# Kernel tuning notes

Measured on AMD Instinct MI355X. Metric: run time of the kernel, lower is better.

## Reference

```python
import jax, jax.numpy as jnp
import numpy as np
from jax import lax

B, S, D = 2, 1024, 1024
N = 16            # mamba state dim
EXPAND = 2
DI = EXPAND * D   # inner dim 2048
K = 4             # depthwise conv kernel
H = 16            # soliton heads
DH = D // H
DT_RANK = D // 16
SOL_DT = 0.1      # soliton integration step


def _ln(x, g, b):
    mu = jnp.mean(x, -1, keepdims=True)
    var = jnp.var(x, -1, keepdims=True)
    return (x - mu) / jnp.sqrt(var + 1e-5) * g + b


def setup_inputs() -> dict:
    key = jax.random.key(0)
    ks = jax.random.split(key, 12)
    def nrm(k, sh, sc=0.02):
        return jax.random.normal(k, sh, jnp.float32) * sc
    return {
        'x': nrm(ks[0], (B, S, D), 1.0),
        'ln1_g': jnp.ones(D), 'ln1_b': jnp.zeros(D),
        'W_in': nrm(ks[1], (D, 2 * DI)), 'b_in': jnp.zeros(2 * DI),
        'conv_w': nrm(ks[2], (DI, K), 0.1), 'conv_b': jnp.zeros(DI),
        'W_xp': nrm(ks[3], (DI, DT_RANK + 2 * N)),
        'W_dt': nrm(ks[4], (DT_RANK, DI), 0.1),
        'b_dt': jnp.full((DI,), -4.6),  # softplus(-4.6) ~ 0.01 init dt
        'A_log': jnp.log(jnp.broadcast_to(jnp.arange(1, N + 1, dtype=jnp.float32), (DI, N))),
        'D_skip': jnp.ones(DI),
        'W_out': nrm(ks[5], (DI, D)), 'b_out': jnp.zeros(D),
        'ln2_g': jnp.ones(D), 'ln2_b': jnp.zeros(D),
        'W_si': nrm(ks[6], (D, D)), 'b_si': jnp.zeros(D),
        'gates': nrm(ks[7], (H, 3), 0.1),   # per-head weights for [sine-Gordon, KdV, Heimburg-Jackson]
        'alpha': nrm(ks[8], (H,), 0.1),     # HJ nonlinearity coefficient
        'W_so': nrm(ks[9], (D, D)), 'b_so': jnp.zeros(D),
    }


def _forward(x, ln1_g, ln1_b, W_in, b_in, conv_w, conv_b, W_xp, W_dt, b_dt,
             A_log, D_skip, W_out, b_out, ln2_g, ln2_b, W_si, b_si,
             gates, alpha, W_so, b_so):
    b, s, d = x.shape
    # ---- Mamba mixer branch ----
    u = _ln(x, ln1_g, ln1_b)
    xz = u @ W_in + b_in                                   # [b,s,2*DI]
    xp, z = jnp.split(xz, 2, axis=-1)                      # [b,s,DI] each
    # causal depthwise conv along sequence
    xt = xp.transpose(0, 2, 1)                             # [b,DI,s]
    yc = lax.conv_general_dilated(xt, conv_w[:, None, :], (1,), [(K - 1, 0)],
                                  feature_group_count=DI,
                                  dimension_numbers=('NCW', 'OIW', 'NCW'))
    xc = jax.nn.silu(yc.transpose(0, 2, 1) + conv_b)       # [b,s,DI]
    dbc = xc @ W_xp
    dtr, Bs, Cs = jnp.split(dbc, [DT_RANK, DT_RANK + N], axis=-1)
    dt = jax.nn.softplus(dtr @ W_dt + b_dt)                # [b,s,DI]
    A = -jnp.exp(A_log)                                    # [DI,N]
    dA = jnp.exp(dt[..., None] * A)                        # [b,s,DI,N]
    dBx = (dt * xc)[..., None] * Bs[:, :, None, :]         # [b,s,DI,N]

    def step(h, inp):
        dA_t, dBx_t, C_t = inp
        h = dA_t * h + dBx_t                               # [b,DI,N]
        y = jnp.einsum('bdn,bn->bd', h, C_t)
        return h, y

    h0 = jnp.zeros((b, DI, N), x.dtype)
    xs = (dA.transpose(1, 0, 2, 3), dBx.transpose(1, 0, 2, 3), Cs.transpose(1, 0, 2))
    _, ys = lax.scan(step, h0, xs)
    y = ys.transpose(1, 0, 2)                              # [b,s,DI]
    y = (y + xc * D_skip) * jax.nn.silu(z)
    x = x + y @ W_out + b_out

    # ---- Soliton interaction branch ----
    v = _ln(x, ln2_g, ln2_b)
    uu = (v @ W_si + b_si).reshape(b, s, H, DH)
    up = jnp.pad(uu, ((0, 0), (2, 2), (0, 0), (0, 0)), mode='edge')
    ux = (up[:, 3:-1] - up[:, 1:-3]) * 0.5                 # central 1st derivative
    uxx = up[:, 3:-1] - 2.0 * uu + up[:, 1:-3]
    uxxx = (up[:, 4:] - 2.0 * up[:, 3:-1] + 2.0 * up[:, 1:-3] - up[:, :-4]) * 0.5
    sg = jnp.sin(uu)                                       # sine-Gordon
    kdv = -6.0 * uu * ux - uxxx                            # KdV
    hj = (1.0 + alpha[None, None, :, None] * uu) * uxx     # Heimburg-Jackson
    du = (gates[None, None, :, 0:1] * sg
          + gates[None, None, :, 1:2] * kdv
          + gates[None, None, :, 2:3] * hj)
    sol = (SOL_DT * du).reshape(b, s, d) @ W_so + b_so
    return x + sol


def reference(x, ln1_g, ln1_b, W_in, b_in, conv_w, conv_b, W_xp, W_dt, b_dt,
              A_log, D_skip, W_out, b_out, ln2_g, ln2_b, W_si, b_si,
              gates, alpha, W_so, b_so):
    return _forward(x, ln1_g, ln1_b, W_in, b_in, conv_w, conv_b, W_xp, W_dt, b_dt,
                    A_log, D_skip, W_out, b_out, ln2_g, ln2_b, W_si, b_si,
                    gates, alpha, W_so, b_so)
```

## Files before the change

### kernel.cpp

```cpp
#include <hip/hip_runtime.h>
#include <hip/hip_bf16.h>
#include <math.h>

typedef unsigned short u16;
typedef unsigned int u32;
typedef __attribute__((ext_vector_type(8))) short short8;
typedef __attribute__((ext_vector_type(4))) float f32x4;

constexpr int CB = 2;
constexpr int CS = 1024;
constexpr int CD = 1024;
constexpr int CDI = 2048;
constexpr int CNC2 = 64;
constexpr int CL2 = 16;

__device__ inline u16 f2bf(float v) {
  __hip_bfloat16 h = __float2bfloat16(v);
  return *reinterpret_cast<u16*>(&h);
}
__device__ inline float bf2f(u16 v) {
  return __uint_as_float(((u32)v) << 16);
}

__device__ inline void gload16(const void* g, void* l) {
  __builtin_amdgcn_global_load_lds((const __attribute__((address_space(1))) void*)g,
                                   (__attribute__((address_space(3))) void*)l, 16, 0, 0);
}

struct TJob { const float* src; u16* dst; int K, N, gx, base; };
struct TJobs { TJob j[6]; };

__global__ __launch_bounds__(256)
void transpose_all_kernel(TJobs jobs) {
  int b = blockIdx.x;
  int ji = 0;
#pragma unroll
  for (int i = 1; i < 6; ++i) if (b >= jobs.j[i].base) ji = i;
  TJob jb = jobs.j[ji];
  int lb = b - jb.base;
  int n0 = (lb % jb.gx) * 32, k0 = (lb / jb.gx) * 32;
  __shared__ float tile[32][33];
  int tx = threadIdx.x & 31, ty = threadIdx.x >> 5;
#pragma unroll
  for (int i = 0; i < 4; ++i) {
    int k = k0 + ty + i * 8, n = n0 + tx;
    tile[ty + i * 8][tx] = (n < jb.N) ? jb.src[(size_t)k * jb.N + n] : 0.f;
  }
  __syncthreads();
#pragma unroll
  for (int i = 0; i < 4; ++i) {
    int n = n0 + ty + i * 8, k = k0 + tx;
    jb.dst[(size_t)n * jb.K + k] = f2bf(tile[tx][ty + i * 8]);
  }
}

__global__ __launch_bounds__(256)
void ln_kernel(const float* __restrict__ x, const float* __restrict__ g,
               const float* __restrict__ bb, u16* __restrict__ outb) {
  int row = blockIdx.x;
  const float4* xr = (const float4*)(x + (size_t)row * CD);
  float4 v = xr[threadIdx.x];
  float s = v.x + v.y + v.z + v.w;
  float ss = v.x * v.x + v.y * v.y + v.z * v.z + v.w * v.w;
#pragma unroll
  for (int o = 1; o < 64; o <<= 1) { s += __shfl_xor(s, o); ss += __shfl_xor(ss, o); }
  __shared__ float sb[4], ssb[4];
  int wid = threadIdx.x >> 6;
  if ((threadIdx.x & 63) == 0) { sb[wid] = s; ssb[wid] = ss; }
  __syncthreads();
  s = sb[0] + sb[1] + sb[2] + sb[3];
  ss = ssb[0] + ssb[1] + ssb[2] + ssb[3];
  float mu = s * (1.f / CD);
  float var = ss * (1.f / CD) - mu * mu;
  float rstd = rsqrtf(var + 1e-5f);
  float4 gv = ((const float4*)g)[threadIdx.x];
  float4 bv = ((const float4*)bb)[threadIdx.x];
  ushort4 o;
  o.x = f2bf((v.x - mu) * rstd * gv.x + bv.x);
  o.y = f2bf((v.y - mu) * rstd * gv.y + bv.y);
  o.z = f2bf((v.z - mu) * rstd * gv.z + bv.z);
  o.w = f2bf((v.w - mu) * rstd * gv.w + bv.w);
  ((ushort4*)(outb + (size_t)row * CD))[threadIdx.x] = o;
}

template<int BN, int LDA, int LDB>
__global__ __launch_bounds__(256)
void gemm2_kernel(const u16* __restrict__ A, const u16* __restrict__ Bt,
                  const float* __restrict__ bias,
                  const float* __restrict__ resid, int ldr,
                  float* __restrict__ C, int ldc,
                  u16* __restrict__ aux, int auxN,
                  int Nact, int K, int act) {
  constexpr int WN = BN / 32;
  constexpr int AHALF = 128 * 64;
  constexpr int BHALF = BN * 64;
  __shared__ __align__(16) u16 As[2 * AHALF];
  __shared__ __align__(16) u16 Bs[2 * BHALF];
  const int tid = threadIdx.x, lane = tid & 63, wid = tid >> 6;
  const int wr = wid >> 1, wc = wid & 1;
  int nwg = gridDim.x * gridDim.y;
  int bid = blockIdx.y * gridDim.x + blockIdx.x;
  int swz = (bid & 7) * (nwg >> 3) + (bid >> 3);
  int bx = swz % gridDim.x, by = swz / gridDim.x;
  const int bm = by * 128, bn = bx * BN;
  const int kper = K / gridDim.z;
  const int kbeg = blockIdx.z * kper;
  const int nt = kper / 64;

  int a_src[4], b_src[WN], a_dst[4], b_dst[WN];
#pragma unroll
  for (int j = 0; j < 4; ++j) {
    int c = tid + j * 256;
    int row = c >> 3, kc = (c & 7) ^ (row & 7);
    a_src[j] = (bm + row) * LDA + kc * 8 + kbeg;
    a_dst[j] = (j * 256 + wid * 64) * 8;
  }
#pragma unroll
  for (int j = 0; j < WN; ++j) {
    int c = tid + j * 256;
    int row = c >> 3, kc = (c & 7) ^ (row & 7);
    b_src[j] = (bn + row) * LDB + kc * 8 + kbeg;
    b_dst[j] = (j * 256 + wid * 64) * 8;
  }
  int afo[4], bfo[WN];
#pragma unroll
  for (int m = 0; m < 4; ++m) {
    int r = wr * 64 + m * 16 + (lane & 15);
    afo[m] = r * 64 + (((lane >> 4) ^ (r & 7)) << 3);
  }
#pragma unroll
  for (int n = 0; n < WN; ++n) {
    int r = wc * (BN / 2) + n * 16 + (lane & 15);
    bfo[n] = r * 64 + (((lane >> 4) ^ (r & 7)) << 3);
  }
  f32x4 acc[4][WN] = {};

  auto stage = [&](int t, int abuf, int bbuf) {
    int k0 = t * 64;
#pragma unroll
    for (int j = 0; j < 4; ++j)
      gload16(A + a_src[j] + k0, As + abuf + a_dst[j]);
#pragma unroll
    for (int j = 0; j < WN; ++j)
      gload16(Bt + b_src[j] + k0, Bs + bbuf + b_dst[j]);
  };
  auto compute = [&](int abuf, int bbuf) {
#pragma unroll
    for (int ks = 0; ks < 2; ++ks) {
      short8 af[4], bfr[WN];
#pragma unroll
      for (int m = 0; m < 4; ++m) af[m] = *(const short8*)&As[abuf + (afo[m] ^ (ks * 32))];
#pragma unroll
      for (int n = 0; n < WN; ++n) bfr[n] = *(const short8*)&Bs[bbuf + (bfo[n] ^ (ks * 32))];
#pragma unroll
      for (int m = 0; m < 4; ++m)
#pragma unroll
        for (int n = 0; n < WN; ++n)
          acc[m][n] = __builtin_amdgcn_mfma_f32_16x16x32_bf16(af[m], bfr[n], acc[m][n], 0, 0, 0);
    }
  };

  stage(0, 0, 0);
  __syncthreads();
  int t = 0;
  while (true) {
    if (t + 1 < nt) stage(t + 1, AHALF, BHALF);
    compute(0, 0);
    __syncthreads();
    if (++t == nt) break;
    if (t + 1 < nt) stage(t + 1, 0, 0);
    compute(AHALF, BHALF);
    __syncthreads();
    if (++t == nt) break;
  }

  const int fr = lane & 15, fq = lane >> 4;
  const int ksegs = gridDim.z;
#pragma unroll
  for (int m = 0; m < 4; ++m) {
#pragma unroll
    for (int n = 0; n < WN; ++n) {
#pragma unroll
      for (int j = 0; j < 4; ++j) {
        int row = bm + wr * 64 + m * 16 + fq * 4 + j;
        int col = bn + wc * (BN / 2) + n * 16 + fr;
        if (col < Nact) {
          float v = acc[m][n][j];
          if (ksegs == 1) {
            if (bias) v += bias[col];
            if (resid) v += resid[(size_t)row * ldr + col];
            if (act == 1) v = (v > 20.f) ? v : log1pf(__expf(v));
            if (C) C[(size_t)row * ldc + col] = v;
            if (aux && col < auxN) aux[(size_t)row * auxN + col] = f2bf(v);
          } else {
            atomicAdd(&C[(size_t)row * ldc + col], v);
          }
        }
      }
    }
  }
}

__global__ __launch_bounds__(256)
void conv_silu_kernel(const u16* __restrict__ xz, const float* __restrict__ w,
                      const float* __restrict__ cb, u16* __restrict__ xcb) {
  int idx = blockIdx.x * 256 + threadIdx.x;
  int d = idx & (CDI - 1);
  int t = (idx >> 11) & (CS - 1);
  int b = idx >> 21;
  const u16* col = xz + (size_t)b * CS * 4096 + d;
  float acc = cb[d];
#pragma unroll
  for (int k = 0; k < 4; ++k) {
    int tt = t - 3 + k;
    if (tt >= 0) acc = fmaf(bf2f(col[(size_t)tt * 4096]), w[d * 4 + k], acc);
  }
  float v = acc * (1.f / (1.f + __expf(-acc)));
  xcb[idx] = f2bf(v);
}

__global__ __launch_bounds__(256)
void dtr_convert_kernel(const float* __restrict__ dbc, u16* __restrict__ dtrb) {
  int idx = blockIdx.x * 256 + threadIdx.x;
  int r = idx >> 6, k = idx & 63;
  dtrb[idx] = f2bf(dbc[r * 96 + k]);
}

__global__ __launch_bounds__(256)
void scan1_kernel(const u16* __restrict__ dtb, const u16* __restrict__ xcb,
                  const float* __restrict__ dbc, const float* __restrict__ A_log,
                  u16* __restrict__ P, u16* __restrict__ Q) {
  int gid = blockIdx.x * 256 + threadIdx.x;
  int d = gid & (CDI - 1);
  int c = (gid >> 11) & (CNC2 - 1);
  int b = gid >> 17;
  float acoef[16];
#pragma unroll
  for (int j = 0; j < 4; ++j) {
    float4 al = ((const float4*)(A_log + d * 16))[j];
    acoef[j * 4 + 0] = -__expf(al.x);
    acoef[j * 4 + 1] = -__expf(al.y);
    acoef[j * 4 + 2] = -__expf(al.z);
    acoef[j * 4 + 3] = -__expf(al.w);
  }
  float Pv[16], Qv[16];
#pragma unroll
  for (int n = 0; n < 16; ++n) { Pv[n] = 1.f; Qv[n] = 0.f; }
  size_t rowbase = (size_t)b * CS + (size_t)c * CL2;
  for (int i = 0; i < CL2; ++i) {
    size_t r = rowbase + i;
    float dtv = bf2f(dtb[r * CDI + d]);
    float xcv = bf2f(xcb[r * CDI + d]);
    float dx = dtv * xcv;
    const float4* bs4 = (const float4*)(dbc + r * 96 + 64);
    float bs[16];
#pragma unroll
    for (int j = 0; j < 4; ++j) {
      float4 t4 = bs4[j];
      bs[j * 4 + 0] = t4.x; bs[j * 4 + 1] = t4.y; bs[j * 4 + 2] = t4.z; bs[j * 4 + 3] = t4.w;
    }
#pragma unroll
    for (int n = 0; n < 16; ++n) {
      float a = __expf(dtv * acoef[n]);
      Pv[n] *= a;
      Qv[n] = fmaf(a, Qv[n], dx * bs[n]);
    }
  }
  size_t o = (((size_t)b * CNC2 + c) * CDI + d) * 16;
  u16 pb[16], qb[16];
#pragma unroll
  for (int n = 0; n < 16; ++n) { pb[n] = f2bf(Pv[n]); qb[n] = f2bf(Qv[n]); }
#pragma unroll
  for (int j = 0; j < 2; ++j) {
    *(short8*)(P + o + j * 8) = *(short8*)(pb + j * 8);
    *(short8*)(Q + o + j * 8) = *(short8*)(qb + j * 8);
  }
}

__global__ __launch_bounds__(256)
void scan2_kernel(const u16* __restrict__ P, u16* __restrict__ Q) {
  int gid = blockIdx.x * 256 + threadIdx.x;
  int n = gid & 15;
  int d = (gid >> 4) & (CDI - 1);
  int b = gid >> 15;
  int obase = ((b * CNC2) * CDI + d) * 16 + n;
  constexpr int CSTRIDE = CDI * 16;
  float h = 0.f;
  for (int c0 = 0; c0 < CNC2; c0 += 8) {
    float pv[8], qv[8];
#pragma unroll
    for (int i = 0; i < 8; ++i) {
      int o = obase + (c0 + i) * CSTRIDE;
      pv[i] = bf2f(P[o]);
      qv[i] = bf2f(Q[o]);
    }
#pragma unroll
    for (int i = 0; i < 8; ++i) {
      int o = obase + (c0 + i) * CSTRIDE;
      Q[o] = f2bf(h);
      h = fmaf(pv[i], h, qv[i]);
    }
  }
}

__global__ __launch_bounds__(256)
void scan3_kernel(const u16* __restrict__ dtb, const u16* __restrict__ xcb,
                  const float* __restrict__ dbc, const float* __restrict__ A_log,
                  const u16* __restrict__ Q, const u16* __restrict__ xz,
                  const float* __restrict__ Dskip, u16* __restrict__ y2b) {
  int gid = blockIdx.x * 256 + threadIdx.x;
  int d = gid & (CDI - 1);
  int c = (gid >> 11) & (CNC2 - 1);
  int b = gid >> 17;
  float acoef[16];
#pragma unroll
  for (int j = 0; j < 4; ++j) {
    float4 al = ((const float4*)(A_log + d * 16))[j];
    acoef[j * 4 + 0] = -__expf(al.x);
    acoef[j * 4 + 1] = -__expf(al.y);
    acoef[j * 4 + 2] = -__expf(al.z);
    acoef[j * 4 + 3] = -__expf(al.w);
  }
  float h[16];
  size_t o = (((size_t)b * CNC2 + c) * CDI + d) * 16;
#pragma unroll
  for (int j = 0; j < 2; ++j) {
    short8 q8 = *(const short8*)(Q + o + j * 8);
#pragma unroll
    for (int n = 0; n < 8; ++n) h[j * 8 + n] = bf2f((u16)q8[n]);
  }
  float dsk = Dskip[d];
  size_t rowbase = (size_t)b * CS + (size_t)c * CL2;
  for (int i = 0; i < CL2; ++i) {
    size_t r = rowbase + i;
    float dtv = bf2f(dtb[r * CDI + d]);
    float xcv = bf2f(xcb[r * CDI + d]);
    float zv = bf2f(xz[r * 4096 + 2048 + d]);
    float dx = dtv * xcv;
    const float4* bc4 = (const float4*)(dbc + r * 96 + 64);
    float bs[16], cs[16];
#pragma unroll
    for (int j = 0; j < 4; ++j) {
      float4 t4 = bc4[j];
      bs[j * 4 + 0] = t4.x; bs[j * 4 + 1] = t4.y; bs[j * 4 + 2] = t4.z; bs[j * 4 + 3] = t4.w;
      float4 u4 = bc4[4 + j];
      cs[j * 4 + 0] = u4.x; cs[j * 4 + 1] = u4.y; cs[j * 4 + 2] = u4.z; cs[j * 4 + 3] = u4.w;
    }
    float y = 0.f;
#pragma unroll
    for (int n = 0; n < 16; ++n) {
      float a = __expf(dtv * acoef[n]);
      h[n] = fmaf(a, h[n], dx * bs[n]);
      y = fmaf(h[n], cs[n], y);
    }
    float sz = zv * (1.f / (1.f + __expf(-zv)));
    y2b[r * CDI + d] = f2bf((y + xcv * dsk) * sz);
  }
}

__global__ __launch_bounds__(256)
void soliton_kernel(const float* __restrict__ uu, const float* __restrict__ gates,
                    const float* __restrict__ alpha, u16* __restrict__ sol) {
  int idx = blockIdx.x * 256 + threadIdx.x;
  int d = idx & (CD - 1);
  int t = (idx >> 10) & (CS - 1);
  int b = idx >> 20;
  int h = d >> 6;
  const float* base = uu + (size_t)b * CS * CD + d;
  int tm2 = max(t - 2, 0), tm1 = max(t - 1, 0);
  int tp1 = min(t + 1, CS - 1), tp2 = min(t + 2, CS - 1);
  float um2 = base[(size_t)tm2 * CD];
  float um1 = base[(size_t)tm1 * CD];
  float u0  = base[(size_t)t   * CD];
  float up1 = base[(size_t)tp1 * CD];
  float up2 = base[(size_t)tp2 * CD];
  float ux   = (up1 - um1) * 0.5f;
  float uxx  = up1 - 2.f * u0 + um1;
  float uxxx = (up2 - 2.f * up1 + 2.f * um1 - um2) * 0.5f;
  float sg = sinf(u0);
  float kdv = -6.f * u0 * ux - uxxx;
  float hj = (1.f + alpha[h] * u0) * uxx;
  float du = gates[h * 3 + 0] * sg + gates[h * 3 + 1] * kdv + gates[h * 3 + 2] * hj;
  sol[idx] = f2bf(0.1f * du);
}

extern "C" void kernel_launch(void* const* d_in, const int* in_sizes, int n_in,
                              void* d_out, int out_size, void* d_ws, size_t ws_size,
                              hipStream_t stream) {
  const float* x      = (const float*)d_in[0];
  const float* ln1_g  = (const float*)d_in[1];
  const float* ln1_b  = (const float*)d_in[2];
  const float* W_in   = (const float*)d_in[3];
  const float* b_in   = (const float*)d_in[4];
  const float* conv_w = (const float*)d_in[5];
  const float* conv_b = (const float*)d_in[6];
  const float* W_xp   = (const float*)d_in[7];
  const float* W_dt   = (const float*)d_in[8];
  const float* b_dt   = (const float*)d_in[9];
  const float* A_log  = (const float*)d_in[10];
  const float* D_skip = (const float*)d_in[11];
  const float* W_out  = (const float*)d_in[12];
  const float* b_out  = (const float*)d_in[13];
  const float* ln2_g  = (const float*)d_in[14];
  const float* ln2_b  = (const float*)d_in[15];
  const float* W_si   = (const float*)d_in[16];
  const float* b_si   = (const float*)d_in[17];
  const float* gates  = (const float*)d_in[18];
  const float* alpha  = (const float*)d_in[19];
  const float* W_so   = (const float*)d_in[20];
  const float* b_so   = (const float*)d_in[21];
  float* out = (float*)d_out;

  float* ws = (float*)d_ws;
  size_t off = 0;
  auto alloc = [&](size_t nwords) { float* p = ws + off; off += nwords; return p; };
  const size_t BS = (size_t)CB * CS;
  const size_t M1 = 1024 * 1024;

  u16* Wt_in  = (u16*)alloc(2 * M1);
  u16* Wt_xp  = (u16*)alloc(128 * 1024);
  u16* Wt_dt  = (u16*)alloc(64 * 1024);
  u16* Wt_out = (u16*)alloc(M1);
  u16* Wt_si  = (u16*)alloc(M1 / 2);
  u16* Wt_so  = (u16*)alloc(M1 / 2);
  u16* u_bf   = (u16*)alloc(M1);
  u16* sol_bf = u_bf;
  u16* xz_bf  = (u16*)alloc(4 * M1);
  u16* dt_bf  = (u16*)alloc(2 * M1);
  u16* xc_bf  = (u16*)alloc(2 * M1);
  float* dbc  = alloc(BS * 96);
  u16* dtr_bf = (u16*)alloc(64 * 1024);
  u16* Pb     = (u16*)alloc(2 * M1);
  u16* Qb     = (u16*)alloc(2 * M1);
  u16* y2_bf  = (u16*)alloc(2 * M1);
  float* uu   = (float*)Pb;

  dim3 blk(256);

  {
    TJobs jobs;
    int base = 0;
    auto mk = [&](const float* s, u16* dst, int K, int N) {
      int gx = (N + 31) / 32, gy = K / 32;
      TJob j{s, dst, K, N, gx, base};
      base += gx * gy;
      return j;
    };
    jobs.j[0] = mk(W_in, Wt_in, 1024, 4096);
    jobs.j[1] = mk(W_xp, Wt_xp, 2048, 96);
    jobs.j[2] = mk(W_dt, Wt_dt, 64, 2048);
    jobs.j[3] = mk(W_out, Wt_out, 2048, 1024);
    jobs.j[4] = mk(W_si, Wt_si, 1024, 1024);
    jobs.j[5] = mk(W_so, Wt_so, 1024, 1024);
    hipMemsetAsync(Wt_xp, 0, 128 * 2048 * sizeof(u16), stream);
    transpose_all_kernel<<<base, blk, 0, stream>>>(jobs);
  }

  ln_kernel<<<BS, blk, 0, stream>>>(x, ln1_g, ln1_b, u_bf);
  gemm2_kernel<128, 1024, 1024><<<dim3(32, 16), blk, 0, stream>>>(
      u_bf, Wt_in, b_in, nullptr, 0, nullptr, 0, xz_bf, 4096, 4096, 1024, 0);
  conv_silu_kernel<<<(BS * CDI) / 256, blk, 0, stream>>>(xz_bf, conv_w, conv_b, xc_bf);
  hipMemsetAsync(dbc, 0, BS * 96 * sizeof(float), stream);
  gemm2_kernel<128, 2048, 2048><<<dim3(1, 16, 8), blk, 0, stream>>>(
      xc_bf, Wt_xp, nullptr, nullptr, 0, dbc, 96, nullptr, 0, 96, 2048, 0);
  dtr_convert_kernel<<<(BS * 64) / 256, blk, 0, stream>>>(dbc, dtr_bf);
  gemm2_kernel<128, 64, 64><<<dim3(16, 16), blk, 0, stream>>>(
      dtr_bf, Wt_dt, b_dt, nullptr, 0, nullptr, 0, dt_bf, 2048, 2048, 64, 1);
  scan1_kernel<<<(CB * CNC2 * CDI) / 256, blk, 0, stream>>>(dt_bf, xc_bf, dbc, A_log, Pb, Qb);
  scan2_kernel<<<(CB * CDI * 16) / 256, blk, 0, stream>>>(Pb, Qb);
  scan3_kernel<<<(CB * CNC2 * CDI) / 256, blk, 0, stream>>>(dt_bf, xc_bf, dbc, A_log, Qb, xz_bf, D_skip, y2_bf);
  gemm2_kernel<64, 2048, 2048><<<dim3(16, 16), blk, 0, stream>>>(
      y2_bf, Wt_out, b_out, x, 1024, out, CD, nullptr, 0, 1024, 2048, 0);
  ln_kernel<<<BS, blk, 0, stream>>>(out, ln2_g, ln2_b, u_bf);
  gemm2_kernel<64, 1024, 1024><<<dim3(16, 16), blk, 0, stream>>>(
      u_bf, Wt_si, b_si, nullptr, 0, uu, CD, nullptr, 0, 1024, 1024, 0);
  soliton_kernel<<<(BS * CD) / 256, blk, 0, stream>>>(uu, gates, alpha, sol_bf);
  gemm2_kernel<64, 1024, 1024><<<dim3(16, 16), blk, 0, stream>>>(
      sol_bf, Wt_so, b_so, out, 1024, out, CD, nullptr, 0, 1024, 1024, 0);
}
```

Baseline: 286.8 us.

## Halve GEMM K-tile, add split-K for small GEMMs, vectorize conv, fuse residual+LN

Result: slower. 305.2 us (+6.4%).

```diff
diff --git a/kernel.cpp b/kernel.cpp
--- a/kernel.cpp
+++ b/kernel.cpp
@@ -83,17 +83,55 @@
   ((ushort4*)(outb + (size_t)row * CD))[threadIdx.x] = o;
 }
 
+__global__ __launch_bounds__(256)
+void ln_fuse_kernel(const float* __restrict__ x, const float* __restrict__ S,
+                    const float* __restrict__ bo, const float* __restrict__ g,
+                    const float* __restrict__ bb, float* __restrict__ out,
+                    u16* __restrict__ outb) {
+  int row = blockIdx.x;
+  float4 xv = ((const float4*)(x + (size_t)row * CD))[threadIdx.x];
+  float4 sv = ((const float4*)(S + (size_t)row * CD))[threadIdx.x];
+  float4 bv0 = ((const float4*)bo)[threadIdx.x];
+  float4 v;
+  v.x = xv.x + sv.x + bv0.x;
+  v.y = xv.y + sv.y + bv0.y;
+  v.z = xv.z + sv.z + bv0.z;
+  v.w = xv.w + sv.w + bv0.w;
+  ((float4*)(out + (size_t)row * CD))[threadIdx.x] = v;
+  float s = v.x + v.y + v.z + v.w;
+  float ss = v.x * v.x + v.y * v.y + v.z * v.z + v.w * v.w;
+#pragma unroll
+  for (int o = 1; o < 64; o <<= 1) { s += __shfl_xor(s, o); ss += __shfl_xor(ss, o); }
+  __shared__ float sb[4], ssb[4];
+  int wid = threadIdx.x >> 6;
+  if ((threadIdx.x & 63) == 0) { sb[wid] = s; ssb[wid] = ss; }
+  __syncthreads();
+  s = sb[0] + sb[1] + sb[2] + sb[3];
+  ss = ssb[0] + ssb[1] + ssb[2] + ssb[3];
+  float mu = s * (1.f / CD);
+  float var = ss * (1.f / CD) - mu * mu;
+  float rstd = rsqrtf(var + 1e-5f);
+  float4 gv = ((const float4*)g)[threadIdx.x];
+  float4 bv = ((const float4*)bb)[threadIdx.x];
+  ushort4 o;
+  o.x = f2bf((v.x - mu) * rstd * gv.x + bv.x);
+  o.y = f2bf((v.y - mu) * rstd * gv.y + bv.y);
+  o.z = f2bf((v.z - mu) * rstd * gv.z + bv.z);
+  o.w = f2bf((v.w - mu) * rstd * gv.w + bv.w);
+  ((ushort4*)(outb + (size_t)row * CD))[threadIdx.x] = o;
+}
+
 template<int BN, int LDA, int LDB>
 __global__ __launch_bounds__(256)
-void gemm2_kernel(const u16* __restrict__ A, const u16* __restrict__ Bt,
+void gemm3_kernel(const u16* __restrict__ A, const u16* __restrict__ Bt,
                   const float* __restrict__ bias,
                   const float* __restrict__ resid, int ldr,
                   float* __restrict__ C, int ldc,
                   u16* __restrict__ aux, int auxN,
                   int Nact, int K, int act) {
   constexpr int WN = BN / 32;
-  constexpr int AHALF = 128 * 64;
-  constexpr int BHALF = BN * 64;
+  constexpr int AHALF = 128 * 32;
+  constexpr int BHALF = BN * 32;
   __shared__ __align__(16) u16 As[2 * AHALF];
   __shared__ __align__(16) u16 Bs[2 * BHALF];
   const int tid = threadIdx.x, lane = tid & 63, wid = tid >> 6;
@@ -105,59 +143,55 @@
   const int bm = by * 128, bn = bx * BN;
   const int kper = K / gridDim.z;
   const int kbeg = blockIdx.z * kper;
-  const int nt = kper / 64;
-
-  int a_src[4], b_src[WN], a_dst[4], b_dst[WN];
-#pragma unroll
-  for (int j = 0; j < 4; ++j) {
+  const int nt = kper / 32;
+
+  int a_src[2], b_src[WN / 2 + 1];
+#pragma unroll
+  for (int j = 0; j < 2; ++j) {
     int c = tid + j * 256;
-    int row = c >> 3, kc = (c & 7) ^ (row & 7);
+    int row = c >> 2, kc = (c & 3) ^ (row & 3);
     a_src[j] = (bm + row) * LDA + kc * 8 + kbeg;
-    a_dst[j] = (j * 256 + wid * 64) * 8;
-  }
-#pragma unroll
-  for (int j = 0; j < WN; ++j) {
+  }
+#pragma unroll
+  for (int j = 0; j < BN / 64; ++j) {
     int c = tid + j * 256;
-    int row = c >> 3, kc = (c & 7) ^ (row & 7);
+    int row = c >> 2, kc = (c & 3) ^ (row & 3);
     b_src[j] = (bn + row) * LDB + kc * 8 + kbeg;
-    b_dst[j] = (j * 256 + wid * 64) * 8;
   }
   int afo[4], bfo[WN];
+  const int ch = lane >> 4;
 #pragma unroll
   for (int m = 0; m < 4; ++m) {
     int r = wr * 64 + m * 16 + (lane & 15);
-    afo[m] = r * 64 + (((lane >> 4) ^ (r & 7)) << 3);
+    afo[m] = r * 32 + ((ch ^ (r & 3)) << 3);
   }
 #pragma unroll
   for (int n = 0; n < WN; ++n) {
     int r = wc * (BN / 2) + n * 16 + (lane & 15);
-    bfo[n] = r * 64 + (((lane >> 4) ^ (r & 7)) << 3);
+    bfo[n] = r * 32 + ((ch ^ (r & 3)) << 3);
   }
   f32x4 acc[4][WN] = {};
 
   auto stage = [&](int t, int abuf, int bbuf) {
-    int k0 = t * 64;
-#pragma unroll
-    for (int j = 0; j < 4; ++j)
-      gload16(A + a_src[j] + k0, As + abuf + a_dst[j]);
-#pragma unroll
-    for (int j = 0; j < WN; ++j)
-      gload16(Bt + b_src[j] + k0, Bs + bbuf + b_dst[j]);
+    int k0 = t * 32;
+#pragma unroll
+    for (int j = 0; j < 2; ++j)
+      gload16(A + a_src[j] + k0, As + abuf + (tid + j * 256) * 8);
+#pragma unroll
+    for (int j = 0; j < BN / 64; ++j)
+      gload16(Bt + b_src[j] + k0, Bs + bbuf + (tid + j * 256) * 8);
   };
   auto compute = [&](int abuf, int bbuf) {
-#pragma unroll
-    for (int ks = 0; ks < 2; ++ks) {
-      short8 af[4], bfr[WN];
-#pragma unroll
-      for (int m = 0; m < 4; ++m) af[m] = *(const short8*)&As[abuf + (afo[m] ^ (ks * 32))];
-#pragma unroll
-      for (int n = 0; n < WN; ++n) bfr[n] = *(const short8*)&Bs[bbuf + (bfo[n] ^ (ks * 32))];
-#pragma unroll
-      for (int m = 0; m < 4; ++m)
-#pragma unroll
-        for (int n = 0; n < WN; ++n)
-          acc[m][n] = __builtin_amdgcn_mfma_f32_16x16x32_bf16(af[m], bfr[n], acc[m][n], 0, 0, 0);
-    }
+    short8 af[4], bfr[WN];
+#pragma unroll
+    for (int m = 0; m < 4; ++m) af[m] = *(const short8*)&As[abuf + afo[m]];
+#pragma unroll
+    for (int n = 0; n < WN; ++n) bfr[n] = *(const short8*)&Bs[bbuf + bfo[n]];
+#pragma unroll
+    for (int m = 0; m < 4; ++m)
+#pragma unroll
+      for (int n = 0; n < WN; ++n)
+        acc[m][n] = __builtin_amdgcn_mfma_f32_16x16x32_bf16(af[m], bfr[n], acc[m][n], 0, 0, 0);
   };
 
   stage(0, 0, 0);
@@ -205,18 +239,31 @@
 void conv_silu_kernel(const u16* __restrict__ xz, const float* __restrict__ w,
                       const float* __restrict__ cb, u16* __restrict__ xcb) {
   int idx = blockIdx.x * 256 + threadIdx.x;
-  int d = idx & (CDI - 1);
-  int t = (idx >> 11) & (CS - 1);
-  int b = idx >> 21;
-  const u16* col = xz + (size_t)b * CS * 4096 + d;
-  float acc = cb[d];
+  int d0 = (idx & 255) * 8;
+  int t = (idx >> 8) & (CS - 1);
+  int b = idx >> 18;
+  const u16* base = xz + (size_t)(b * CS) * 4096 + d0;
+  float acc[8];
+  float4 cb2[2] = { ((const float4*)(cb + d0))[0], ((const float4*)(cb + d0))[1] };
+#pragma unroll
+  for (int i = 0; i < 8; ++i) acc[i] = ((const float*)cb2)[i];
 #pragma unroll
   for (int k = 0; k < 4; ++k) {
     int tt = t - 3 + k;
-    if (tt >= 0) acc = fmaf(bf2f(col[(size_t)tt * 4096]), w[d * 4 + k], acc);
-  }
-  float v = acc * (1.f / (1.f + __expf(-acc)));
-  xcb[idx] = f2bf(v);
+    if (tt >= 0) {
+      short8 v = *(const short8*)(base + (size_t)tt * 4096);
+#pragma unroll
+      for (int i = 0; i < 8; ++i)
+        acc[i] = fmaf(bf2f((u16)v[i]), w[(d0 + i) * 4 + k], acc[i]);
+    }
+  }
+  short8 o;
+#pragma unroll
+  for (int i = 0; i < 8; ++i) {
+    float v = acc[i] * (1.f / (1.f + __expf(-acc[i])));
+    o[i] = (short)f2bf(v);
+  }
+  *(short8*)(xcb + (size_t)(b * CS + t) * CDI + d0) = o;
 }
 
 __global__ __launch_bounds__(256)
@@ -359,23 +406,25 @@
 }
 
 __global__ __launch_bounds__(256)
-void soliton_kernel(const float* __restrict__ uu, const float* __restrict__ gates,
-                    const float* __restrict__ alpha, u16* __restrict__ sol) {
+void soliton_kernel(const float* __restrict__ uuraw, const float* __restrict__ bsi,
+                    const float* __restrict__ gates, const float* __restrict__ alpha,
+                    u16* __restrict__ sol) {
   int idx = blockIdx.x * 256 + threadIdx.x;
   int d = idx & (CD - 1);
   int t = (idx >> 10) & (CS - 1);
   int b = idx >> 20;
   int h = d >> 6;
-  const float* base = uu + (size_t)b * CS * CD + d;
+  const float* base = uuraw + (size_t)b * CS * CD + d;
   int tm2 = max(t - 2, 0), tm1 = max(t - 1, 0);
   int tp1 = min(t + 1, CS - 1), tp2 = min(t + 2, CS - 1);
   float um2 = base[(size_t)tm2 * CD];
   float um1 = base[(size_t)tm1 * CD];
-  float u0  = base[(size_t)t   * CD];
+  float u0r = base[(size_t)t   * CD];
   float up1 = base[(size_t)tp1 * CD];
   float up2 = base[(size_t)tp2 * CD];
+  float u0 = u0r + bsi[d];
   float ux   = (up1 - um1) * 0.5f;
-  float uxx  = up1 - 2.f * u0 + um1;
+  float uxx  = up1 - 2.f * u0r + um1;
   float uxxx = (up2 - 2.f * up1 + 2.f * um1 - um2) * 0.5f;
   float sg = sinf(u0);
   float kdv = -6.f * u0 * ux - uxxx;
@@ -430,10 +479,13 @@
   u16* xc_bf  = (u16*)alloc(2 * M1);
   float* dbc  = alloc(BS * 96);
   u16* dtr_bf = (u16*)alloc(64 * 1024);
-  u16* Pb     = (u16*)alloc(2 * M1);
-  u16* Qb     = (u16*)alloc(2 * M1);
+  float* Pb_f = alloc(2 * M1);
+  float* Qb_f = alloc(2 * M1);
+  u16* Pb = (u16*)Pb_f;
+  u16* Qb = (u16*)Qb_f;
+  float* S  = Pb_f;
+  float* S2 = Qb_f;
   u16* y2_bf  = (u16*)alloc(2 * M1);
-  float* uu   = (float*)Pb;
 
   dim3 blk(256);
 
@@ -457,24 +509,26 @@
   }
 
   ln_kernel<<<BS, blk, 0, stream>>>(x, ln1_g, ln1_b, u_bf);
-  gemm2_kernel<128, 1024, 1024><<<dim3(32, 16), blk, 0, stream>>>(
+  gemm3_kernel<64, 1024, 1024><<<dim3(64, 16), blk, 0, stream>>>(
       u_bf, Wt_in, b_in, nullptr, 0, nullptr, 0, xz_bf, 4096, 4096, 1024, 0);
-  conv_silu_kernel<<<(BS * CDI) / 256, blk, 0, stream>>>(xz_bf, conv_w, conv_b, xc_bf);
+  conv_silu_kernel<<<(BS * CDI) / (256 * 8), blk, 0, stream>>>(xz_bf, conv_w, conv_b, xc_bf);
   hipMemsetAsync(dbc, 0, BS * 96 * sizeof(float), stream);
-  gemm2_kernel<128, 2048, 2048><<<dim3(1, 16, 8), blk, 0, stream>>>(
+  gemm3_kernel<128, 2048, 2048><<<dim3(1, 16, 16), blk, 0, stream>>>(
       xc_bf, Wt_xp, nullptr, nullptr, 0, dbc, 96, nullptr, 0, 96, 2048, 0);
   dtr_convert_kernel<<<(BS * 64) / 256, blk, 0, stream>>>(dbc, dtr_bf);
-  gemm2_kernel<128, 64, 64><<<dim3(16, 16), blk, 0, stream>>>(
+  gemm3_kernel<128, 64, 64><<<dim3(16, 16), blk, 0, stream>>>(
       dtr_bf, Wt_dt, b_dt, nullptr, 0, nullptr, 0, dt_bf, 2048, 2048, 64, 1);
   scan1_kernel<<<(CB * CNC2 * CDI) / 256, blk, 0, stream>>>(dt_bf, xc_bf, dbc, A_log, Pb, Qb);
   scan2_kernel<<<(CB * CDI * 16) / 256, blk, 0, stream>>>(Pb, Qb);
   scan3_kernel<<<(CB * CNC2 * CDI) / 256, blk, 0, stream>>>(dt_bf, xc_bf, dbc, A_log, Qb, xz_bf, D_skip, y2_bf);
-  gemm2_kernel<64, 2048, 2048><<<dim3(16, 16), blk, 0, stream>>>(
-      y2_bf, Wt_out, b_out, x, 1024, out, CD, nullptr, 0, 1024, 2048, 0);
-  ln_kernel<<<BS, blk, 0, stream>>>(out, ln2_g, ln2_b, u_bf);
-  gemm2_kernel<64, 1024, 1024><<<dim3(16, 16), blk, 0, stream>>>(
-      u_bf, Wt_si, b_si, nullptr, 0, uu, CD, nullptr, 0, 1024, 1024, 0);
-  soliton_kernel<<<(BS * CD) / 256, blk, 0, stream>>>(uu, gates, alpha, sol_bf);
-  gemm2_kernel<64, 1024, 1024><<<dim3(16, 16), blk, 0, stream>>>(
+  hipMemsetAsync(S, 0, BS * CD * sizeof(float), stream);
+  gemm3_kernel<64, 2048, 2048><<<dim3(16, 16, 2), blk, 0, stream>>>(
+      y2_bf, Wt_out, nullptr, nullptr, 0, S, CD, nullptr, 0, 1024, 2048, 0);
+  ln_fuse_kernel<<<BS, blk, 0, stream>>>(x, S, b_out, ln2_g, ln2_b, out, u_bf);
+  hipMemsetAsync(S2, 0, BS * CD * sizeof(float), stream);
+  gemm3_kernel<64, 1024, 1024><<<dim3(16, 16, 2), blk, 0, stream>>>(
+      u_bf, Wt_si, nullptr, nullptr, 0, S2, CD, nullptr, 0, 1024, 1024, 0);
+  soliton_kernel<<<(BS * CD) / 256, blk, 0, stream>>>(S2, b_si, gates, alpha, sol_bf);
+  gemm3_kernel<64, 1024, 1024><<<dim3(16, 16), blk, 0, stream>>>(
       sol_bf, Wt_so, b_so, out, 1024, out, CD, nullptr, 0, 1024, 1024, 0);
 }
```
